# Performance work log

Measured on AMD Instinct MI355X. Metric: run time of the kernel, lower is better.

Reference implementation:

```python
import math
import jax
import jax.numpy as jnp
import numpy as np
from jax import lax

B_, L, D_MODEL = 2, 1024, 2048
D_STATE, D_CONV, EXPAND = 16, 4, 2
D_INNER = EXPAND * D_MODEL          # 4096
DT_RANK = math.ceil(D_MODEL / 16)   # 128


def setup_inputs() -> dict:
    key = jax.random.key(0)
    ks = jax.random.split(key, 8)
    hidden_states = jax.random.normal(ks[0], (B_, L, D_MODEL), jnp.float32)
    in_proj_w = jax.random.normal(ks[1], (2 * D_INNER, D_MODEL), jnp.float32) * (D_MODEL ** -0.5)
    conv_w = jax.random.normal(ks[2], (D_INNER, D_CONV), jnp.float32) * (D_CONV ** -0.5)
    conv_b = jnp.zeros((D_INNER,), jnp.float32)
    x_proj_w = jax.random.normal(ks[3], (DT_RANK + 2 * D_STATE, D_INNER), jnp.float32) * (D_INNER ** -0.5)
    dt_std = DT_RANK ** -0.5
    dt_proj_w = jax.random.uniform(ks[4], (D_INNER, DT_RANK), jnp.float32, minval=-dt_std, maxval=dt_std)
    # dt bias init: softplus^{-1} of dt sampled log-uniform in [1e-3, 1e-1]
    dt = jnp.exp(jax.random.uniform(ks[5], (D_INNER,), jnp.float32)
                 * (math.log(0.1) - math.log(0.001)) + math.log(0.001))
    dt = jnp.clip(dt, 1e-4)
    dt_proj_b = dt + jnp.log(-jnp.expm1(-dt))
    A_log = jnp.log(jnp.broadcast_to(jnp.arange(1, D_STATE + 1, dtype=jnp.float32), (D_INNER, D_STATE)))
    D = jnp.ones((D_INNER,), jnp.float32)
    out_proj_w = jax.random.normal(ks[6], (D_MODEL, D_INNER), jnp.float32) * (D_INNER ** -0.5)
    return {
        'hidden_states': hidden_states, 'in_proj_w': in_proj_w,
        'conv_w': conv_w, 'conv_b': conv_b, 'x_proj_w': x_proj_w,
        'dt_proj_w': dt_proj_w, 'dt_proj_b': dt_proj_b,
        'A_log': A_log, 'D': D, 'out_proj_w': out_proj_w,
    }


def _silu(v):
    return v * jax.nn.sigmoid(v)


def _mamba_forward(hidden_states, in_proj_w, conv_w, conv_b, x_proj_w,
                   dt_proj_w, dt_proj_b, A_log, D, out_proj_w):
    b, l, _ = hidden_states.shape
    # in_proj: (b,l,d_model) -> (b, 2*d_inner, l)
    xz = jnp.einsum('bld,ed->bel', hidden_states, in_proj_w)
    x, z = xz[:, :D_INNER, :], xz[:, D_INNER:, :]
    A = -jnp.exp(A_log.astype(jnp.float32))  # (d_inner, d_state)
    # causal depthwise conv1d + SiLU
    xp = jnp.pad(x, ((0, 0), (0, 0), (D_CONV - 1, 0)))
    x = lax.conv_general_dilated(
        xp, conv_w[:, None, :], window_strides=(1,), padding='VALID',
        dimension_numbers=('NCH', 'OIH', 'NCH'), feature_group_count=D_INNER)
    x = _silu(x + conv_b[None, :, None])  # (b, d_inner, l)
    # x_proj -> dt, B, C
    x_dbl = jnp.einsum('bdl,kd->blk', x, x_proj_w)  # (b,l,dt_rank+2n)
    dt_lo = x_dbl[..., :DT_RANK]
    Bmat = x_dbl[..., DT_RANK:DT_RANK + D_STATE]          # (b,l,n)
    Cmat = x_dbl[..., DT_RANK + D_STATE:]                 # (b,l,n)
    delta = jax.nn.softplus(jnp.einsum('blr,dr->bld', dt_lo, dt_proj_w)
                            + dt_proj_b.astype(jnp.float32))  # (b,l,d)
    xt = jnp.transpose(x, (2, 0, 1))       # (l,b,d)
    dl = jnp.transpose(delta, (1, 0, 2))   # (l,b,d)
    Bl = jnp.transpose(Bmat, (1, 0, 2))    # (l,b,n)
    Cl = jnp.transpose(Cmat, (1, 0, 2))    # (l,b,n)

    def step(h, inp):
        d_t, B_t, C_t, x_t = inp
        dA = jnp.exp(d_t[..., None] * A)                       # (b,d,n)
        h = h * dA + d_t[..., None] * B_t[:, None, :] * x_t[..., None]
        y_t = jnp.sum(h * C_t[:, None, :], axis=-1)            # (b,d)
        return h, y_t

    h0 = jnp.zeros((b, D_INNER, D_STATE), jnp.float32)
    _, ys = lax.scan(step, h0, (dl, Bl, Cl, xt))  # ys: (l,b,d)
    y = jnp.transpose(ys, (1, 0, 2))              # (b,l,d)
    y = y + jnp.transpose(x, (0, 2, 1)) * D[None, None, :]
    y = y * _silu(jnp.transpose(z, (0, 2, 1)))
    out = jnp.einsum('bld,ed->ble', y, out_proj_w)  # (b,l,d_model)
    return out


def reference(hidden_states, in_proj_w, conv_w, conv_b, x_proj_w,
              dt_proj_w, dt_proj_b, A_log, D, out_proj_w):
    return _mamba_forward(hidden_states, in_proj_w, conv_w, conv_b, x_proj_w,
                          dt_proj_w, dt_proj_b, A_log, D, out_proj_w)
```

## Files before the change

kernel.cpp:

```cpp
#include <hip/hip_runtime.h>
#include <hip/hip_bf16.h>
#include <stdint.h>

#define BB 2
#define LL 1024
#define DMODEL 2048
#define DINNER 4096
#define DSTATE 16
#define DTRANK 128
#define XDBL_LD 256
#define CHUNK 64
#define NCH (LL / CHUNK)

typedef unsigned short ushort;
using short8 = __attribute__((ext_vector_type(8))) short;
using f32x4  = __attribute__((ext_vector_type(4))) float;
using us4    = __attribute__((ext_vector_type(4))) ushort;

__device__ __forceinline__ float bf2f(ushort u) {
    union { uint32_t i; float f; } v; v.i = ((uint32_t)u) << 16; return v.f;
}
__device__ __forceinline__ ushort f2bf(float f) {
    union { float f; uint32_t i; } v; v.f = f;
    uint32_t lsb = (v.i >> 16) & 1u;
    uint32_t r = v.i + 0x7FFFu + lsb;
    return (ushort)(r >> 16);
}

__device__ __forceinline__ void glds16(const ushort* g, ushort* l) {
    __builtin_amdgcn_global_load_lds(
        (const __attribute__((address_space(1))) void*)g,
        (__attribute__((address_space(3))) void*)l,
        16, 0, 0);
}

__global__ __launch_bounds__(256) void cvt_all(
    const float4* __restrict__ hidden, const float4* __restrict__ inproj,
    const float4* __restrict__ dtw, const float4* __restrict__ outp,
    const float4* __restrict__ xproj,
    us4* __restrict__ hid_h, us4* __restrict__ inp_h, us4* __restrict__ dtp_h,
    us4* __restrict__ outp_h, us4* __restrict__ xpp)
{
    long i = (long)blockIdx.x * 256 + threadIdx.x;
    const float4* src; us4* dst; long j;
    if (i < 1048576)      { src = hidden; dst = hid_h;  j = i; }
    else if (i < 5242880) { src = inproj; dst = inp_h;  j = i - 1048576; }
    else if (i < 5373952) { src = dtw;    dst = dtp_h;  j = i - 5242880; }
    else if (i < 7471104) { src = outp;   dst = outp_h; j = i - 5373952; }
    else {
        j = i - 7471104; dst = xpp;
        if (j >= 163840) { us4 z = {0, 0, 0, 0}; dst[j] = z; return; }
        src = xproj;
    }
    float4 v = src[j];
    us4 o; o.x = f2bf(v.x); o.y = f2bf(v.y); o.z = f2bf(v.z); o.w = f2bf(v.w);
    dst[j] = o;
}

template <int EPI, bool WF, bool WH>
__global__ __launch_bounds__(256) void gemm_nt(
    const ushort* __restrict__ A, int lda,
    const ushort* __restrict__ Bm, int ldb,
    float* __restrict__ Cf, ushort* __restrict__ Ch, int ldc,
    int K, const float* __restrict__ bias)
{
    __shared__ __align__(16) ushort sA[128 * 64];
    __shared__ __align__(16) ushort sB[128 * 64];

    const int tid  = threadIdx.x;
    const int lane = tid & 63;
    const int wave = tid >> 6;
    const int wr = wave >> 1, wc = wave & 1;

    const int NT = gridDim.x, MT = gridDim.y;
    int mt, nt;
    if ((NT & 7) == 0) {
        int lin   = blockIdx.y * NT + blockIdx.x;
        int strip = NT >> 3;
        int xcd   = lin & 7;
        int idx   = lin >> 3;
        nt = xcd * strip + (idx % strip);
        mt = idx / strip;
    } else { mt = blockIdx.y; nt = blockIdx.x; }
    const long m0 = (long)mt * 128;
    const long n0 = (long)nt * 128;

    const long zoff = (long)blockIdx.z;
    A  += zoff * (long)K;
    Bm += zoff * (long)K;
    const long Mrows = (long)MT * 128;
    if (WF) Cf += zoff * Mrows * (long)ldc;
    if (WH) Ch += zoff * Mrows * (long)ldc;

    f32x4 acc[4][4] = {};

    const int lrow = lane & 15;
    const int q    = lane >> 4;

    const int sr  = tid >> 3;
    const int scb = (tid & 7) ^ (sr & 7);
    const int sc  = scb << 3;
    const ushort* Ag = A  + (m0 + sr) * (long)lda + sc;
    const ushort* Bg = Bm + (n0 + sr) * (long)ldb + sc;
    ushort* lA = sA + tid * 8;
    ushort* lB = sB + tid * 8;

    for (int k0 = 0; k0 < K; k0 += 64) {
        __syncthreads();
        #pragma unroll
        for (int c = 0; c < 4; ++c) {
            glds16(Ag + (c * 32) * (long)lda + k0, lA + c * 2048);
            glds16(Bg + (c * 32) * (long)ldb + k0, lB + c * 2048);
        }
        __syncthreads();

        #pragma unroll
        for (int ks = 0; ks < 2; ++ks) {
            const int off = (((ks * 4 + q) ^ (lrow & 7)) << 3);
            short8 af[4], bf[4];
            #pragma unroll
            for (int i = 0; i < 4; ++i)
                af[i] = *(const short8*)&sA[(wr * 64 + i * 16 + lrow) * 64 + off];
            #pragma unroll
            for (int j = 0; j < 4; ++j)
                bf[j] = *(const short8*)&sB[(wc * 64 + j * 16 + lrow) * 64 + off];

            #pragma unroll
            for (int i = 0; i < 4; ++i)
                #pragma unroll
                for (int j = 0; j < 4; ++j)
                    acc[i][j] = __builtin_amdgcn_mfma_f32_16x16x32_bf16(
                        af[i], bf[j], acc[i][j], 0, 0, 0);
        }
    }

    const int r0 = q * 4;
    const int c0 = lane & 15;
    #pragma unroll
    for (int i = 0; i < 4; ++i) {
        #pragma unroll
        for (int j = 0; j < 4; ++j) {
            long col = n0 + wc * 64 + j * 16 + c0;
            float bv = 0.f;
            if (EPI == 1) bv = bias[col];
            #pragma unroll
            for (int r = 0; r < 4; ++r) {
                long row = m0 + wr * 64 + i * 16 + r0 + r;
                float v = acc[i][j][r];
                if (EPI == 1) {
                    v += bv;
                    v = (v > 20.f) ? v : log1pf(__expf(v));
                }
                long idx = row * (long)ldc + col;
                if (WF) Cf[idx] = v;
                if (WH) Ch[idx] = f2bf(v);
            }
        }
    }
}

template <int NZ, bool WH_>
__global__ __launch_bounds__(256) void reduce_k(
    const float4* __restrict__ parts, long stride4, int n4,
    float4* __restrict__ outF, us4* __restrict__ outH)
{
    int i = blockIdx.x * 256 + threadIdx.x;
    if (i >= n4) return;
    float4 s = parts[i];
    #pragma unroll
    for (int z = 1; z < NZ; ++z) {
        float4 v = parts[(long)z * stride4 + i];
        s.x += v.x; s.y += v.y; s.z += v.z; s.w += v.w;
    }
    if (outF) outF[i] = s;
    if (WH_) {
        us4 o; o.x = f2bf(s.x); o.y = f2bf(s.y); o.z = f2bf(s.z); o.w = f2bf(s.w);
        outH[i] = o;
    }
}

__global__ __launch_bounds__(256) void conv_silu_kernel(
    const ushort* __restrict__ xz,
    const float* __restrict__ cw,
    const float* __restrict__ cb,
    ushort* __restrict__ xc)
{
    int gid = blockIdx.x * 256 + threadIdx.x;
    int d  = gid & (DINNER - 1);
    int rl = gid >> 12;
    int l  = rl & (LL - 1);
    float acc = cb[d];
    #pragma unroll
    for (int j = 0; j < 4; ++j) {
        int li = l - 3 + j;
        if (li >= 0)
            acc += cw[d * 4 + j] * bf2f(xz[(long)(rl - 3 + j) * 8192 + d]);
    }
    float s = acc / (1.f + __expf(-acc));
    xc[gid] = f2bf(s);
}

__global__ __launch_bounds__(256) void scan_p1(
    const ushort* __restrict__ delta,
    const ushort* __restrict__ xc,
    const float*  __restrict__ xdbl,
    const float*  __restrict__ A_log,
    float* __restrict__ Hbuf,
    float* __restrict__ sumdt_buf)
{
    __shared__ float sB[CHUNK * 16];
    const int tid = threadIdx.x;
    const int k = blockIdx.y, b = blockIdx.z;
    const int d = blockIdx.x * 256 + tid;
    const int row0 = b * LL + k * CHUNK;

    #pragma unroll
    for (int i = 0; i < 4; ++i) {
        int idx = i * 256 + tid;
        sB[idx] = xdbl[(long)(row0 + (idx >> 4)) * XDBL_LD + DTRANK + (idx & 15)];
    }
    __syncthreads();

    float A[DSTATE];
    const float4* Ap = (const float4*)(A_log + d * DSTATE);
    #pragma unroll
    for (int i = 0; i < 4; ++i) {
        float4 v = Ap[i];
        A[i*4+0] = -__expf(v.x); A[i*4+1] = -__expf(v.y);
        A[i*4+2] = -__expf(v.z); A[i*4+3] = -__expf(v.w);
    }

    float H[DSTATE];
    #pragma unroll
    for (int s = 0; s < DSTATE; ++s) H[s] = 0.f;
    float sumdt = 0.f;

    for (int t = 0; t < CHUNK; ++t) {
        const long row = row0 + t;
        const float dt = bf2f(delta[row * DINNER + d]);
        const float xv = bf2f(xc[row * DINNER + d]);
        const float dx = dt * xv;
        sumdt += dt;
        #pragma unroll
        for (int s = 0; s < DSTATE; ++s) {
            float dA = __expf(dt * A[s]);
            H[s] = H[s] * dA + dx * sB[t * 16 + s];
        }
    }

    const long o = ((long)(b * NCH + k) * DINNER + d) * DSTATE;
    float4* Ho = (float4*)(Hbuf + o);
    #pragma unroll
    for (int i = 0; i < 4; ++i) {
        float4 v; v.x = H[i*4+0]; v.y = H[i*4+1]; v.z = H[i*4+2]; v.w = H[i*4+3];
        Ho[i] = v;
    }
    sumdt_buf[(b * NCH + k) * DINNER + d] = sumdt;
}

__global__ __launch_bounds__(256) void scan_p2(
    const float* __restrict__ A_log,
    const float* __restrict__ sumdt_buf,
    float* __restrict__ Hbuf)
{
    int gid = blockIdx.x * 256 + threadIdx.x;
    int b = gid >> 16;
    int rem = gid & 65535;
    int d = rem >> 4, s = rem & 15;
    float A = -__expf(A_log[d * DSTATE + s]);
    float h = 0.f;
    for (int k = 0; k < NCH; ++k) {
        long idx = ((long)(b * NCH + k) * DINNER + d) * DSTATE + s;
        float Hk = Hbuf[idx];
        float sd = sumdt_buf[(b * NCH + k) * DINNER + d];
        Hbuf[idx] = h;
        h = h * __expf(A * sd) + Hk;
    }
}

__global__ __launch_bounds__(256) void scan_p3(
    const ushort* __restrict__ delta,
    const ushort* __restrict__ xc,
    const float*  __restrict__ xdbl,
    const ushort* __restrict__ xz,
    const float*  __restrict__ A_log,
    const float*  __restrict__ Dp,
    const float*  __restrict__ hin,
    ushort* __restrict__ y)
{
    __shared__ float sBC[CHUNK * 32];
    const int tid = threadIdx.x;
    const int k = blockIdx.y, b = blockIdx.z;
    const int d = blockIdx.x * 256 + tid;
    const int row0 = b * LL + k * CHUNK;

    #pragma unroll
    for (int i = 0; i < 8; ++i) {
        int idx = i * 256 + tid;
        sBC[idx] = xdbl[(long)(row0 + (idx >> 5)) * XDBL_LD + DTRANK + (idx & 31)];
    }
    __syncthreads();

    float A[DSTATE];
    const float4* Ap = (const float4*)(A_log + d * DSTATE);
    #pragma unroll
    for (int i = 0; i < 4; ++i) {
        float4 v = Ap[i];
        A[i*4+0] = -__expf(v.x); A[i*4+1] = -__expf(v.y);
        A[i*4+2] = -__expf(v.z); A[i*4+3] = -__expf(v.w);
    }
    const float Dd = Dp[d];

    float h[DSTATE];
    const float4* Hp = (const float4*)(hin + ((long)(b * NCH + k) * DINNER + d) * DSTATE);
    #pragma unroll
    for (int i = 0; i < 4; ++i) {
        float4 v = Hp[i];
        h[i*4+0] = v.x; h[i*4+1] = v.y; h[i*4+2] = v.z; h[i*4+3] = v.w;
    }

    for (int t = 0; t < CHUNK; ++t) {
        const long row = row0 + t;
        const float dt = bf2f(delta[row * DINNER + d]);
        const float xv = bf2f(xc[row * DINNER + d]);
        const float dx = dt * xv;
        float yt = 0.f;
        #pragma unroll
        for (int s = 0; s < DSTATE; ++s) {
            float dA = __expf(dt * A[s]);
            h[s] = h[s] * dA + dx * sBC[t * 32 + s];
            yt += h[s] * sBC[t * 32 + 16 + s];
        }
        yt += xv * Dd;
        const float zv = bf2f(xz[row * 8192 + DINNER + d]);
        yt *= zv / (1.f + __expf(-zv));
        y[row * DINNER + d] = f2bf(yt);
    }
}

extern "C" void kernel_launch(void* const* d_in, const int* in_sizes, int n_in,
                              void* d_out, int out_size, void* d_ws, size_t ws_size,
                              hipStream_t stream)
{
    const float* hidden    = (const float*)d_in[0];
    const float* in_proj   = (const float*)d_in[1];
    const float* conv_w    = (const float*)d_in[2];
    const float* conv_b    = (const float*)d_in[3];
    const float* x_proj    = (const float*)d_in[4];
    const float* dt_proj_w = (const float*)d_in[5];
    const float* dt_proj_b = (const float*)d_in[6];
    const float* A_log     = (const float*)d_in[7];
    const float* Dp        = (const float*)d_in[8];
    const float* out_proj  = (const float*)d_in[9];
    float* out = (float*)d_out;

    char* ws = (char*)d_ws;
    ushort* xz_h    = (ushort*)(ws);
    ushort* xc      = (ushort*)(ws + 33554432);
    ushort* xpp     = (ushort*)(ws + 50331648);
    float*  xdbl    = (float*)(ws + 52428800);
    ushort* xdblh   = (ushort*)(ws + 54525952);
    ushort* delta_h = (ushort*)(ws + 55574528);
    ushort* yb      = (ushort*)(ws + 72351744);
    ushort* hid_h   = (ushort*)(ws + 89128960);
    ushort* inp_h   = (ushort*)(ws + 97517568);
    float*  parts   = (float*)(ws + 97517568);
    float*  Hbuf    = (float*)(ws + 97517568);
    float*  sumdt   = (float*)(ws + 105906176);
    ushort* dtp_h   = (ushort*)(ws + 131072000);
    ushort* outp_h  = (ushort*)(ws + 132120576);
    float*  parts2  = (float*)(ws);

    const int M = BB * LL;

    cvt_all<<<30208, 256, 0, stream>>>(
        (const float4*)hidden, (const float4*)in_proj, (const float4*)dt_proj_w,
        (const float4*)out_proj, (const float4*)x_proj,
        (us4*)hid_h, (us4*)inp_h, (us4*)dtp_h, (us4*)outp_h, (us4*)xpp);

    gemm_nt<0, false, true><<<dim3(8192 / 128, M / 128), 256, 0, stream>>>(
        hid_h, DMODEL, inp_h, DMODEL, nullptr, xz_h, 8192, DMODEL, nullptr);

    conv_silu_kernel<<<(M * DINNER) / 256, 256, 0, stream>>>(xz_h, conv_w, conv_b, xc);

    gemm_nt<0, true, false><<<dim3(XDBL_LD / 128, M / 128, 16), 256, 0, stream>>>(
        xc, DINNER, xpp, DINNER, parts, nullptr, XDBL_LD, DINNER / 16, nullptr);
    reduce_k<16, true><<<(M * XDBL_LD / 4 + 255) / 256, 256, 0, stream>>>(
        (const float4*)parts, (long)M * XDBL_LD / 4, M * XDBL_LD / 4,
        (float4*)xdbl, (us4*)xdblh);

    gemm_nt<1, false, true><<<dim3(DINNER / 128, M / 128), 256, 0, stream>>>(
        xdblh, XDBL_LD, dtp_h, DTRANK, nullptr, delta_h, DINNER, DTRANK, dt_proj_b);

    scan_p1<<<dim3(DINNER / 256, NCH, BB), 256, 0, stream>>>(
        delta_h, xc, xdbl, A_log, Hbuf, sumdt);
    scan_p2<<<(BB * DINNER * DSTATE) / 256, 256, 0, stream>>>(
        A_log, sumdt, Hbuf);
    scan_p3<<<dim3(DINNER / 256, NCH, BB), 256, 0, stream>>>(
        delta_h, xc, xdbl, xz_h, A_log, Dp, Hbuf, yb);

    gemm_nt<0, true, false><<<dim3(DMODEL / 128, M / 128, 4), 256, 0, stream>>>(
        yb, DINNER, outp_h, DINNER, parts2, nullptr, DMODEL, DINNER / 4, nullptr);
    reduce_k<4, false><<<(M * DMODEL / 4 + 255) / 256, 256, 0, stream>>>(
        (const float4*)parts2, (long)M * DMODEL / 4, M * DMODEL / 4,
        (float4*)out, nullptr);
}
```

Measured before the change: 521.9 us.

## Replace split-K x_proj GEMM and dt_proj GEMM with small-tile MFMA kernels

The x_proj projection previously ran as a 16-way split-K tiled GEMM followed by a reduction kernel. It is replaced by a skinny kernel where each wave computes a 16x16 tile over the full K directly from global memory, which removes the partial-sum buffer and the extra launch. The dt_proj GEMM with its softplus epilogue is also replaced by a dedicated 64x64-tile kernel without LDS staging. The trade-off is that operands are no longer shared through LDS, so global reads are uncoalesced and repeated, and each wave now runs a long serial K loop.

```diff
diff --git a/kernel.cpp b/kernel.cpp
--- a/kernel.cpp
+++ b/kernel.cpp
@@ -159,6 +159,81 @@
     }
 }
 
+__global__ __launch_bounds__(256) void gemm_skinny(
+    const ushort* __restrict__ A, int lda,
+    const ushort* __restrict__ Bm, int ldb,
+    float* __restrict__ Cf, ushort* __restrict__ Ch, int ldc, int K)
+{
+    const int tid  = threadIdx.x;
+    const int lane = tid & 63;
+    const int w    = tid >> 6;
+    const int lrow = lane & 15;
+    const int q    = lane >> 4;
+    const long m0 = (long)blockIdx.y * 64 + w * 16;
+    const long n0 = (long)blockIdx.x * 16;
+
+    const ushort* Ap = A  + (m0 + lrow) * (long)lda + q * 8;
+    const ushort* Bp = Bm + (n0 + lrow) * (long)ldb + q * 8;
+
+    f32x4 acc = {};
+    for (int k0 = 0; k0 < K; k0 += 128) {
+        #pragma unroll
+        for (int u = 0; u < 4; ++u) {
+            short8 af = *(const short8*)(Ap + k0 + u * 32);
+            short8 bf = *(const short8*)(Bp + k0 + u * 32);
+            acc = __builtin_amdgcn_mfma_f32_16x16x32_bf16(af, bf, acc, 0, 0, 0);
+        }
+    }
+
+    #pragma unroll
+    for (int r = 0; r < 4; ++r) {
+        long idx = (m0 + q * 4 + r) * (long)ldc + n0 + lrow;
+        Cf[idx] = acc[r];
+        Ch[idx] = f2bf(acc[r]);
+    }
+}
+
+__global__ __launch_bounds__(256) void gemm_delta(
+    const ushort* __restrict__ A,
+    const ushort* __restrict__ Bm,
+    const float* __restrict__ bias,
+    ushort* __restrict__ Ch)
+{
+    const int tid  = threadIdx.x;
+    const int lane = tid & 63;
+    const int w    = tid >> 6;
+    const int lrow = lane & 15;
+    const int q    = lane >> 4;
+    const long m0 = (long)blockIdx.y * 64 + w * 16;
+    const long n0 = (long)blockIdx.x * 64;
+
+    const ushort* Ap = A  + (m0 + lrow) * (long)XDBL_LD + q * 8;
+    const ushort* Bp = Bm + (n0 + lrow) * (long)DTRANK + q * 8;
+
+    f32x4 acc[4] = {};
+    #pragma unroll
+    for (int ks = 0; ks < 4; ++ks) {
+        short8 af = *(const short8*)(Ap + ks * 32);
+        #pragma unroll
+        for (int j = 0; j < 4; ++j) {
+            short8 bf = *(const short8*)(Bp + j * 16 * DTRANK + ks * 32);
+            acc[j] = __builtin_amdgcn_mfma_f32_16x16x32_bf16(af, bf, acc[j], 0, 0, 0);
+        }
+    }
+
+    #pragma unroll
+    for (int j = 0; j < 4; ++j) {
+        long col = n0 + j * 16 + lrow;
+        float bv = bias[col];
+        #pragma unroll
+        for (int r = 0; r < 4; ++r) {
+            float v = acc[j][r] + bv;
+            v = (v > 20.f) ? v : log1pf(__expf(v));
+            Ch[(m0 + q * 4 + r) * (long)DINNER + col] = f2bf(v);
+        }
+    }
+}
+
 template <int NZ, bool WH_>
 __global__ __launch_bounds__(256) void reduce_k(
     const float4* __restrict__ parts, long stride4, int n4,
@@ -364,7 +439,6 @@
     ushort* yb      = (ushort*)(ws + 72351744);
     ushort* hid_h   = (ushort*)(ws + 89128960);
     ushort* inp_h   = (ushort*)(ws + 97517568);
-    float*  parts   = (float*)(ws + 97517568);
     float*  Hbuf    = (float*)(ws + 97517568);
     float*  sumdt   = (float*)(ws + 105906176);
     ushort* dtp_h   = (ushort*)(ws + 131072000);
@@ -383,14 +457,11 @@
 
     conv_silu_kernel<<<(M * DINNER) / 256, 256, 0, stream>>>(xz_h, conv_w, conv_b, xc);
 
-    gemm_nt<0, true, false><<<dim3(XDBL_LD / 128, M / 128, 16), 256, 0, stream>>>(
-        xc, DINNER, xpp, DINNER, parts, nullptr, XDBL_LD, DINNER / 16, nullptr);
-    reduce_k<16, true><<<(M * XDBL_LD / 4 + 255) / 256, 256, 0, stream>>>(
-        (const float4*)parts, (long)M * XDBL_LD / 4, M * XDBL_LD / 4,
-        (float4*)xdbl, (us4*)xdblh);
-
-    gemm_nt<1, false, true><<<dim3(DINNER / 128, M / 128), 256, 0, stream>>>(
-        xdblh, XDBL_LD, dtp_h, DTRANK, nullptr, delta_h, DINNER, DTRANK, dt_proj_b);
+    gemm_skinny<<<dim3(XDBL_LD / 16, M / 64), 256, 0, stream>>>(
+        xc, DINNER, xpp, DINNER, xdbl, xdblh, XDBL_LD, DINNER);
+
+    gemm_delta<<<dim3(DINNER / 64, M / 64), 256, 0, stream>>>(
+        xdblh, dtp_h, dt_proj_b, delta_h);
 
     scan_p1<<<dim3(DINNER / 256, NCH, BB), 256, 0, stream>>>(
         delta_h, xc, xdbl, A_log, Hbuf, sumdt);
```

After: 538.0 us. 1.03x slower.
